# Kernel tuning notes

Hardware: AMD Instinct MI355X
Metric: run time of the kernel (lower is better)

## Reference

```python
import jax, jax.numpy as jnp
import numpy as np

N, D_IN, D_HID, N_EXPERTS, TOP_K = 16384, 2048, 2048, 8, 2


def setup_inputs() -> dict:
    key = jax.random.key(0)
    k1, k2, k3, k4, k5 = jax.random.split(key, 5)
    x = jax.random.normal(k1, (N, D_IN), dtype=jnp.float32)
    W_experts = jax.random.normal(k2, (N_EXPERTS, D_IN, D_HID), dtype=jnp.float32) * 0.02
    b_experts = jax.random.normal(k3, (N_EXPERTS, D_HID), dtype=jnp.float32) * 0.02
    W_gate = jax.random.normal(k4, (D_IN, N_EXPERTS), dtype=jnp.float32) * 0.02
    b_gate = jax.random.normal(k5, (N_EXPERTS,), dtype=jnp.float32) * 0.02
    return {"x": x, "W_experts": W_experts, "b_experts": b_experts,
            "W_gate": W_gate, "b_gate": b_gate}


def reference(x, W_experts, b_experts, W_gate, b_gate):
    # gating softmax over experts: [N, E]
    gates = jax.nn.softmax(x @ W_gate + b_gate, axis=-1)
    # per-token top-k scores/indices: [N, K]
    top_scores, top_idx = jax.lax.top_k(gates, TOP_K)
    # FAITHFUL to original: experts chosen by the FIRST token's indices for all tokens
    idx0 = top_idx[0]                       # [K]
    W_sel = W_experts[idx0]                 # [K, D_IN, D_HID]
    b_sel = b_experts[idx0]                 # [K, D_HID]
    expert_out = jnp.einsum('ni,kio->nko', x, W_sel) + b_sel[None]  # [N, K, D_HID]
    # weight by each token's own top-k scores and sum over the K experts
    return (expert_out * top_scores[:, :, None]).sum(axis=1)        # [N, D_HID]
```

## Files before the change

### kernel.cpp

```cpp
#include <hip/hip_runtime.h>
#include <hip/hip_bf16.h>
#include <stdint.h>

#define N_TOK 16384
#define D_IN  2048
#define D_HID 2048

typedef __attribute__((ext_vector_type(8))) short  bf16x8;
typedef __attribute__((ext_vector_type(4))) float  f32x4;
typedef __attribute__((ext_vector_type(8))) unsigned short u16x8;

__device__ __forceinline__ unsigned short f2bf(float f) {
    unsigned int u = __float_as_uint(f);
    u = (u + 0x7FFFu + ((u >> 16) & 1u)) >> 16;
    return (unsigned short)u;
}

__global__ void gate_kernel(const float* __restrict__ x,
                            const float* __restrict__ Wg,
                            const float* __restrict__ bg,
                            float* __restrict__ s12,
                            int* __restrict__ eidx) {
    const int token = blockIdx.x * 4 + (threadIdx.x >> 6);
    const int lane  = threadIdx.x & 63;
    const float* xr = x + (size_t)token * D_IN;

    float acc[8];
#pragma unroll
    for (int e = 0; e < 8; ++e) acc[e] = 0.f;

    for (int i = lane; i < D_IN; i += 64) {
        float xv = xr[i];
        const float4* wr = (const float4*)(Wg + (size_t)i * 8);
        float4 w0 = wr[0], w1 = wr[1];
        acc[0] += xv * w0.x; acc[1] += xv * w0.y;
        acc[2] += xv * w0.z; acc[3] += xv * w0.w;
        acc[4] += xv * w1.x; acc[5] += xv * w1.y;
        acc[6] += xv * w1.z; acc[7] += xv * w1.w;
    }
#pragma unroll
    for (int off = 32; off > 0; off >>= 1) {
#pragma unroll
        for (int e = 0; e < 8; ++e) acc[e] += __shfl_xor(acc[e], off);
    }

    float lg[8];
    float mx = -1e30f;
#pragma unroll
    for (int e = 0; e < 8; ++e) { lg[e] = acc[e] + bg[e]; mx = fmaxf(mx, lg[e]); }
    float sum = 0.f;
#pragma unroll
    for (int e = 0; e < 8; ++e) { lg[e] = expf(lg[e] - mx); sum += lg[e]; }
    float inv = 1.f / sum;

    float s1 = -1.f, s2 = -1.f; int i1 = 0, i2 = 0;
#pragma unroll
    for (int e = 0; e < 8; ++e) {
        float g = lg[e] * inv;
        if (g > s1)      { s2 = s1; i2 = i1; s1 = g; i1 = e; }
        else if (g > s2) { s2 = g;  i2 = e; }
    }
    if (lane == 0) {
        s12[token * 2]     = s1;
        s12[token * 2 + 1] = s2;
        if (token == 0) { eidx[0] = i1; eidx[1] = i2; }
    }
}

__global__ __launch_bounds__(256) void xconv_kernel(
    const float* __restrict__ x, unsigned short* __restrict__ xb) {
    const int mt = blockIdx.x >> 6;
    const int kt = blockIdx.x & 63;
    const int t  = threadIdx.x;
    const float* src = x + ((size_t)(mt * 256 + t)) * D_IN + kt * 32;
    unsigned short* slab = xb + ((size_t)(mt * 64 + kt)) * 8192;
#pragma unroll
    for (int ks = 0; ks < 4; ++ks) {
        float4 a = *(const float4*)(src + ks * 8);
        float4 b = *(const float4*)(src + ks * 8 + 4);
        u16x8 v;
        v[0] = f2bf(a.x); v[1] = f2bf(a.y); v[2] = f2bf(a.z); v[3] = f2bf(a.w);
        v[4] = f2bf(b.x); v[5] = f2bf(b.y); v[6] = f2bf(b.z); v[7] = f2bf(b.w);
        *(u16x8*)(slab + (ks * 256 + t) * 8) = v;
    }
}

__global__ void wconv_kernel(const float* __restrict__ W,
                             const int* __restrict__ eidx,
                             unsigned short* __restrict__ wbT) {
    __shared__ float tile[64][65];
    const int be  = blockIdx.z;
    const int e   = eidx[be];
    const int k0  = blockIdx.y * 64;
    const int n0  = blockIdx.x * 64;
    const int bx  = n0 >> 7;
    const int cl0 = n0 & 127;
    const int kt0 = k0 >> 5;
    const float* src = W + (size_t)e * D_IN * D_HID;
    const int t = threadIdx.x;

#pragma unroll
    for (int p = 0; p < 4; ++p) {
        int row = p * 16 + (t >> 4);
        int col = (t & 15) * 4;
        const float* s = src + (size_t)(k0 + row) * D_HID + n0 + col;
        tile[row][col]     = s[0];
        tile[row][col + 1] = s[1];
        tile[row][col + 2] = s[2];
        tile[row][col + 3] = s[3];
    }
    __syncthreads();

    const int g   = (t >> 5) * 8;
    const int ktl = t >> 7;
    const int ks  = (t >> 5) & 3;
#pragma unroll
    for (int p = 0; p < 2; ++p) {
        int n = p * 32 + (t & 31);
        u16x8 v;
#pragma unroll
        for (int j = 0; j < 8; ++j) v[j] = f2bf(tile[g + j][n]);
        unsigned short* dst = wbT + ((size_t)(bx * 64 + kt0 + ktl)) * 8192 +
                              ((size_t)(ks * 256 + be * 128 + cl0 + n)) * 8;
        *(u16x8*)dst = v;
    }
}

#define GLD16(gp, lp)                                                        \
    __builtin_amdgcn_global_load_lds(                                        \
        (const __attribute__((address_space(1))) void*)(gp),                 \
        (__attribute__((address_space(3))) void*)(lp), 16, 0, 0)

#define LDSV(SLOT) (*(const bf16x8*)&lds[(SLOT) * 8])

#define STAGE_A(SBAS, KT)                                                    \
    do {                                                                     \
        GLD16(gA0 + (size_t)(KT) * 8192,        &lds[((SBAS) + t512) * 8]);  \
        GLD16(gA0 + (size_t)(KT) * 8192 + 4096, &lds[((SBAS) + 512 + t512) * 8]); \
    } while (0)
#define STAGE_B(SBAS, KT)                                                    \
    do {                                                                     \
        GLD16(gB0 + (size_t)(KT) * 8192,        &lds[((SBAS) + 1024 + t512) * 8]); \
        GLD16(gB0 + (size_t)(KT) * 8192 + 4096, &lds[((SBAS) + 1536 + t512) * 8]); \
    } while (0)

#define MF(MI, AV)                                                                              \
    acc[MI][0] = __builtin_amdgcn_mfma_f32_16x16x32_bf16(AV, bf0, acc[MI][0], 0, 0, 0);         \
    acc[MI][1] = __builtin_amdgcn_mfma_f32_16x16x32_bf16(AV, bf1, acc[MI][1], 0, 0, 0);         \
    acc[MI][2] = __builtin_amdgcn_mfma_f32_16x16x32_bf16(AV, bf2, acc[MI][2], 0, 0, 0);         \
    acc[MI][3] = __builtin_amdgcn_mfma_f32_16x16x32_bf16(AV, bf3, acc[MI][3], 0, 0, 0);

#define TILE(RB, SB, KT, DO_STAGE, VMSTR)                                    \
    do {                                                                     \
        const int rbas  = (RB) * 2048;                                       \
        const int abase = rbas + aks + arow;                                 \
        const int bbase = rbas + 1024 + aks + brow;                          \
        bf16x8 bf0 = LDSV(bbase), bf1 = LDSV(bbase + 16),                    \
               bf2 = LDSV(bbase + 32), bf3 = LDSV(bbase + 48);               \
        bf16x8 a0 = LDSV(abase), a1 = LDSV(abase + 16),                      \
               a2 = LDSV(abase + 32), a3 = LDSV(abase + 48);                 \
        bf16x8 a4 = LDSV(abase + 64), a5 = LDSV(abase + 80),                 \
               a6 = LDSV(abase + 96), a7 = LDSV(abase + 112);                \
        __builtin_amdgcn_s_barrier();                                        \
        if (DO_STAGE) STAGE_A((SB) * 2048, KT);                              \
        __builtin_amdgcn_s_setprio(1);                                       \
        MF(0, a0) MF(1, a1) MF(2, a2) MF(3, a3)                              \
        __builtin_amdgcn_s_setprio(0);                                       \
        asm volatile(VMSTR ::: "memory");                                    \
        __builtin_amdgcn_s_barrier();                                        \
        if (DO_STAGE) STAGE_B((SB) * 2048, KT);                              \
        __builtin_amdgcn_s_setprio(1);                                       \
        MF(4, a4) MF(5, a5) MF(6, a6) MF(7, a7)                              \
        __builtin_amdgcn_s_setprio(0);                                       \
    } while (0)

__global__ __launch_bounds__(512, 2) void moe_gemm_kernel(
    const unsigned short* __restrict__ xb,
    const unsigned short* __restrict__ wbT,
    const float* __restrict__ b_exp,
    const int* __restrict__ eidx,
    const float* __restrict__ s12,
    float* __restrict__ out) {
    __shared__ __align__(16) short lds[4 * 2048 * 8];

    const int t512 = threadIdx.x;
    const int lane = t512 & 63;
    const int w    = t512 >> 6;
    const int wm   = w >> 2;
    const int wn   = w & 3;

    const int bid = blockIdx.x;
    const int xcd = bid & 7;
    const int jb  = bid >> 3;
    const int bx  = xcd * 2 + (jb & 1);
    const int by  = jb >> 1;
    const int mbase = by * 256;
    const int nbase = bx * 128;

    const unsigned short* gA0 = xb  + ((size_t)by * 64) * 8192 + t512 * 8;
    const unsigned short* gB0 = wbT + ((size_t)bx * 64) * 8192 + t512 * 8;

    const int aks  = (lane >> 4) * 256;
    const int arow = wm * 128 + (lane & 15);
    const int brow = wn * 64 + (lane & 15);

    f32x4 acc[8][4];
#pragma unroll
    for (int mi = 0; mi < 8; ++mi)
#pragma unroll
        for (int ni = 0; ni < 4; ++ni) acc[mi][ni] = (f32x4){0.f, 0.f, 0.f, 0.f};

    STAGE_A(0, 0);    STAGE_B(0, 0);
    STAGE_A(2048, 1); STAGE_B(2048, 1);
    STAGE_A(4096, 2); STAGE_B(4096, 2);
    asm volatile("s_waitcnt vmcnt(8)" ::: "memory");
    __builtin_amdgcn_s_barrier();

#pragma unroll 4
    for (int t = 0; t < 61; ++t) {
        TILE(t & 3, (t + 3) & 3, t + 3, 1, "s_waitcnt vmcnt(6)");
    }
    TILE(1, 0, 0, 0, "s_waitcnt vmcnt(4)");
    TILE(2, 0, 0, 0, "s_waitcnt vmcnt(0)");
    TILE(3, 0, 0, 0, "s_waitcnt vmcnt(0)");

    __syncthreads();
    float* fl = (float*)lds;
    if (wn >= 2) {
        float* reg = fl + (wm * 2 + (wn - 2)) * 8192;
#pragma unroll
        for (int mi = 0; mi < 8; ++mi)
#pragma unroll
            for (int ni = 0; ni < 4; ++ni)
#pragma unroll
                for (int j = 0; j < 4; ++j) {
                    int row_l = mi * 16 + ((lane >> 4) << 2) + j;
                    int col_l = ni * 16 + (lane & 15);
                    reg[row_l * 64 + col_l] = acc[mi][ni][j];
                }
    }
    __syncthreads();
    if (wn < 2) {
        const float* reg = fl + (wm * 2 + wn) * 8192;
        const int e0 = eidx[0], e1 = eidx[1];
        const float* bb0 = b_exp + (size_t)e0 * D_HID;
        const float* bb1 = b_exp + (size_t)e1 * D_HID;
        const float2* s12v = (const float2*)s12;
        int   cc[4];
        float b0c[4], b1c[4];
#pragma unroll
        for (int ni = 0; ni < 4; ++ni) {
            cc[ni]  = nbase + wn * 64 + ni * 16 + (lane & 15);
            b0c[ni] = bb0[cc[ni]];
            b1c[ni] = bb1[cc[ni]];
        }
#pragma unroll
        for (int mi = 0; mi < 8; ++mi)
#pragma unroll
            for (int j = 0; j < 4; ++j) {
                int row_l = mi * 16 + ((lane >> 4) << 2) + j;
                int r = mbase + wm * 128 + row_l;
                float2 s = s12v[r];
#pragma unroll
                for (int ni = 0; ni < 4; ++ni) {
                    float y1 = reg[row_l * 64 + ni * 16 + (lane & 15)];
                    out[(size_t)r * D_HID + cc[ni]] =
                        s.x * (acc[mi][ni][j] + b0c[ni]) + s.y * (y1 + b1c[ni]);
                }
            }
    }
}

extern "C" void kernel_launch(void* const* d_in, const int* in_sizes, int n_in,
                              void* d_out, int out_size, void* d_ws, size_t ws_size,
                              hipStream_t stream) {
    const float* x         = (const float*)d_in[0];
    const float* W_experts = (const float*)d_in[1];
    const float* b_experts = (const float*)d_in[2];
    const float* W_gate    = (const float*)d_in[3];
    const float* b_gate    = (const float*)d_in[4];
    float* out = (float*)d_out;

    char* ws = (char*)d_ws;
    float* s12  = (float*)ws;
    int*   eidx = (int*)(ws + 131072);
    unsigned short* xb  = (unsigned short*)(ws + 262144);
    unsigned short* wbT = (unsigned short*)(ws + 262144 + 67108864);

    gate_kernel<<<N_TOK / 4, 256, 0, stream>>>(x, W_gate, b_gate, s12, eidx);
    xconv_kernel<<<4096, 256, 0, stream>>>(x, xb);
    wconv_kernel<<<dim3(32, 32, 2), 256, 0, stream>>>(W_experts, eidx, wbT);
    moe_gemm_kernel<<<1024, 512, 0, stream>>>(xb, wbT, b_experts, eidx, s12, out);
}
```

Baseline: 323.0 us.

## Fuse gating matvec into x conversion and switch GEMM to 32x32x16 MFMA

The gate logits are now computed as per-k-tile partial sums inside the x-to-bf16 conversion kernel, so x is read once instead of twice. A small finishing kernel reduces the partials, applies softmax and top-2, and writes the scores and expert indices; the partials are staged in the output buffer. Separately, the main GEMM inner loop moves from 16x16x32 to 32x32x16 bf16 MFMA with a 4x2 accumulator tile per wave, which cuts LDS fragment loads per FLOP. The epilogue is remapped to the 32x32 accumulator layout. Risks are higher register pressure from the 16-wide accumulators and the extra partial-sum traffic through the output buffer.

```diff
diff --git a/kernel.cpp b/kernel.cpp
--- a/kernel.cpp
+++ b/kernel.cpp
@@ -6,9 +6,9 @@
 #define D_IN  2048
 #define D_HID 2048
 
-typedef __attribute__((ext_vector_type(8))) short  bf16x8;
-typedef __attribute__((ext_vector_type(4))) float  f32x4;
-typedef __attribute__((ext_vector_type(8))) unsigned short u16x8;
+typedef __attribute__((ext_vector_type(8)))  short bf16x8;
+typedef __attribute__((ext_vector_type(16))) float f32x16;
+typedef __attribute__((ext_vector_type(8)))  unsigned short u16x8;
 
 __device__ __forceinline__ unsigned short f2bf(float f) {
     unsigned int u = __float_as_uint(f);
@@ -16,73 +16,73 @@
     return (unsigned short)u;
 }
 
-__global__ void gate_kernel(const float* __restrict__ x,
-                            const float* __restrict__ Wg,
-                            const float* __restrict__ bg,
-                            float* __restrict__ s12,
-                            int* __restrict__ eidx) {
-    const int token = blockIdx.x * 4 + (threadIdx.x >> 6);
-    const int lane  = threadIdx.x & 63;
-    const float* xr = x + (size_t)token * D_IN;
-
-    float acc[8];
-#pragma unroll
-    for (int e = 0; e < 8; ++e) acc[e] = 0.f;
-
-    for (int i = lane; i < D_IN; i += 64) {
-        float xv = xr[i];
-        const float4* wr = (const float4*)(Wg + (size_t)i * 8);
-        float4 w0 = wr[0], w1 = wr[1];
-        acc[0] += xv * w0.x; acc[1] += xv * w0.y;
-        acc[2] += xv * w0.z; acc[3] += xv * w0.w;
-        acc[4] += xv * w1.x; acc[5] += xv * w1.y;
-        acc[6] += xv * w1.z; acc[7] += xv * w1.w;
-    }
-#pragma unroll
-    for (int off = 32; off > 0; off >>= 1) {
-#pragma unroll
-        for (int e = 0; e < 8; ++e) acc[e] += __shfl_xor(acc[e], off);
-    }
-
-    float lg[8];
-    float mx = -1e30f;
-#pragma unroll
-    for (int e = 0; e < 8; ++e) { lg[e] = acc[e] + bg[e]; mx = fmaxf(mx, lg[e]); }
-    float sum = 0.f;
-#pragma unroll
-    for (int e = 0; e < 8; ++e) { lg[e] = expf(lg[e] - mx); sum += lg[e]; }
-    float inv = 1.f / sum;
-
-    float s1 = -1.f, s2 = -1.f; int i1 = 0, i2 = 0;
-#pragma unroll
-    for (int e = 0; e < 8; ++e) {
-        float g = lg[e] * inv;
-        if (g > s1)      { s2 = s1; i2 = i1; s1 = g; i1 = e; }
-        else if (g > s2) { s2 = g;  i2 = e; }
-    }
-    if (lane == 0) {
-        s12[token * 2]     = s1;
-        s12[token * 2 + 1] = s2;
-        if (token == 0) { eidx[0] = i1; eidx[1] = i2; }
-    }
-}
-
-__global__ __launch_bounds__(256) void xconv_kernel(
-    const float* __restrict__ x, unsigned short* __restrict__ xb) {
+__global__ __launch_bounds__(256) void xconv2_kernel(
+    const float* __restrict__ x, const float* __restrict__ Wg,
+    unsigned short* __restrict__ xb, float* __restrict__ part) {
     const int mt = blockIdx.x >> 6;
     const int kt = blockIdx.x & 63;
     const int t  = threadIdx.x;
     const float* src = x + ((size_t)(mt * 256 + t)) * D_IN + kt * 32;
     unsigned short* slab = xb + ((size_t)(mt * 64 + kt)) * 8192;
+    const float* wg = Wg + kt * 32 * 8;
+
+    float p[8];
+#pragma unroll
+    for (int e = 0; e < 8; ++e) p[e] = 0.f;
+
 #pragma unroll
     for (int ks = 0; ks < 4; ++ks) {
         float4 a = *(const float4*)(src + ks * 8);
         float4 b = *(const float4*)(src + ks * 8 + 4);
+        float xv[8] = {a.x, a.y, a.z, a.w, b.x, b.y, b.z, b.w};
         u16x8 v;
-        v[0] = f2bf(a.x); v[1] = f2bf(a.y); v[2] = f2bf(a.z); v[3] = f2bf(a.w);
-        v[4] = f2bf(b.x); v[5] = f2bf(b.y); v[6] = f2bf(b.z); v[7] = f2bf(b.w);
+#pragma unroll
+        for (int j = 0; j < 8; ++j) v[j] = f2bf(xv[j]);
         *(u16x8*)(slab + (ks * 256 + t) * 8) = v;
-    }
+#pragma unroll
+        for (int j = 0; j < 8; ++j)
+#pragma unroll
+            for (int e = 0; e < 8; ++e)
+                p[e] += xv[j] * wg[(ks * 8 + j) * 8 + e];
+    }
+    float* dst = part + (((size_t)(mt * 64 + kt)) * 256 + t) * 8;
+#pragma unroll
+    for (int e = 0; e < 8; ++e) dst[e] = p[e];
+}
+
+__global__ __launch_bounds__(256) void gatefin_kernel(
+    const float* __restrict__ part, const float* __restrict__ bg,
+    float* __restrict__ s12, int* __restrict__ eidx) {
+    const int mt = blockIdx.x;
+    const int t  = threadIdx.x;
+    float l8[8];
+#pragma unroll
+    for (int e = 0; e < 8; ++e) l8[e] = 0.f;
+    for (int kt = 0; kt < 64; ++kt) {
+        const float* pp = part + (((size_t)(mt * 64 + kt)) * 256 + t) * 8;
+        float4 a = *(const float4*)pp;
+        float4 b = *(const float4*)(pp + 4);
+        l8[0] += a.x; l8[1] += a.y; l8[2] += a.z; l8[3] += a.w;
+        l8[4] += b.x; l8[5] += b.y; l8[6] += b.z; l8[7] += b.w;
+    }
+    float mx = -1e30f;
+#pragma unroll
+    for (int e = 0; e < 8; ++e) { l8[e] += bg[e]; mx = fmaxf(mx, l8[e]); }
+    float sum = 0.f;
+#pragma unroll
+    for (int e = 0; e < 8; ++e) { l8[e] = expf(l8[e] - mx); sum += l8[e]; }
+    float inv = 1.f / sum;
+    float s1 = -1.f, s2 = -1.f; int i1 = 0, i2 = 0;
+#pragma unroll
+    for (int e = 0; e < 8; ++e) {
+        float g = l8[e] * inv;
+        if (g > s1)      { s2 = s1; i2 = i1; s1 = g; i1 = e; }
+        else if (g > s2) { s2 = g;  i2 = e; }
+    }
+    const int token = mt * 256 + t;
+    s12[token * 2]     = s1;
+    s12[token * 2 + 1] = s2;
+    if (token == 0) { eidx[0] = i1; eidx[1] = i2; }
 }
 
 __global__ void wconv_kernel(const float* __restrict__ W,
@@ -144,33 +144,37 @@
         GLD16(gB0 + (size_t)(KT) * 8192 + 4096, &lds[((SBAS) + 1536 + t512) * 8]); \
     } while (0)
 
-#define MF(MI, AV)                                                                              \
-    acc[MI][0] = __builtin_amdgcn_mfma_f32_16x16x32_bf16(AV, bf0, acc[MI][0], 0, 0, 0);         \
-    acc[MI][1] = __builtin_amdgcn_mfma_f32_16x16x32_bf16(AV, bf1, acc[MI][1], 0, 0, 0);         \
-    acc[MI][2] = __builtin_amdgcn_mfma_f32_16x16x32_bf16(AV, bf2, acc[MI][2], 0, 0, 0);         \
-    acc[MI][3] = __builtin_amdgcn_mfma_f32_16x16x32_bf16(AV, bf3, acc[MI][3], 0, 0, 0);
+#define MFC(KK)                                                              \
+    _Pragma("unroll")                                                        \
+    for (int mi = 0; mi < 4; ++mi)                                           \
+        _Pragma("unroll")                                                    \
+        for (int ni = 0; ni < 2; ++ni)                                       \
+            acc[mi][ni] = __builtin_amdgcn_mfma_f32_32x32x16_bf16(           \
+                af[KK][mi], bf[KK][ni], acc[mi][ni], 0, 0, 0);
 
 #define TILE(RB, SB, KT, DO_STAGE, VMSTR)                                    \
     do {                                                                     \
-        const int rbas  = (RB) * 2048;                                       \
-        const int abase = rbas + aks + arow;                                 \
-        const int bbase = rbas + 1024 + aks + brow;                          \
-        bf16x8 bf0 = LDSV(bbase), bf1 = LDSV(bbase + 16),                    \
-               bf2 = LDSV(bbase + 32), bf3 = LDSV(bbase + 48);               \
-        bf16x8 a0 = LDSV(abase), a1 = LDSV(abase + 16),                      \
-               a2 = LDSV(abase + 32), a3 = LDSV(abase + 48);                 \
-        bf16x8 a4 = LDSV(abase + 64), a5 = LDSV(abase + 80),                 \
-               a6 = LDSV(abase + 96), a7 = LDSV(abase + 112);                \
+        const int rbas = (RB) * 2048;                                        \
+        bf16x8 af[2][4], bf[2][2];                                           \
+        _Pragma("unroll")                                                    \
+        for (int kk = 0; kk < 2; ++kk) {                                     \
+            _Pragma("unroll")                                                \
+            for (int ni = 0; ni < 2; ++ni)                                   \
+                bf[kk][ni] = LDSV(rbas + 1024 + kk * 512 + bbase + ni * 32); \
+            _Pragma("unroll")                                                \
+            for (int mi = 0; mi < 4; ++mi)                                   \
+                af[kk][mi] = LDSV(rbas + kk * 512 + abase + mi * 32);        \
+        }                                                                    \
         __builtin_amdgcn_s_barrier();                                        \
         if (DO_STAGE) STAGE_A((SB) * 2048, KT);                              \
         __builtin_amdgcn_s_setprio(1);                                       \
-        MF(0, a0) MF(1, a1) MF(2, a2) MF(3, a3)                              \
+        MFC(0)                                                               \
         __builtin_amdgcn_s_setprio(0);                                       \
         asm volatile(VMSTR ::: "memory");                                    \
         __builtin_amdgcn_s_barrier();                                        \
         if (DO_STAGE) STAGE_B((SB) * 2048, KT);                              \
         __builtin_amdgcn_s_setprio(1);                                       \
-        MF(4, a4) MF(5, a5) MF(6, a6) MF(7, a7)                              \
+        MFC(1)                                                               \
         __builtin_amdgcn_s_setprio(0);                                       \
     } while (0)
 
@@ -188,6 +192,8 @@
     const int w    = t512 >> 6;
     const int wm   = w >> 2;
     const int wn   = w & 3;
+    const int lsk  = lane >> 5;
+    const int lr   = lane & 31;
 
     const int bid = blockIdx.x;
     const int xcd = bid & 7;
@@ -200,15 +206,16 @@
     const unsigned short* gA0 = xb  + ((size_t)by * 64) * 8192 + t512 * 8;
     const unsigned short* gB0 = wbT + ((size_t)bx * 64) * 8192 + t512 * 8;
 
-    const int aks  = (lane >> 4) * 256;
-    const int arow = wm * 128 + (lane & 15);
-    const int brow = wn * 64 + (lane & 15);
-
-    f32x4 acc[8][4];
-#pragma unroll
-    for (int mi = 0; mi < 8; ++mi)
-#pragma unroll
-        for (int ni = 0; ni < 4; ++ni) acc[mi][ni] = (f32x4){0.f, 0.f, 0.f, 0.f};
+    const int abase = lsk * 256 + wm * 128 + lr;
+    const int bbase = lsk * 256 + wn * 64 + lr;
+
+    f32x16 acc[4][2];
+#pragma unroll
+    for (int mi = 0; mi < 4; ++mi)
+#pragma unroll
+        for (int ni = 0; ni < 2; ++ni)
+#pragma unroll
+            for (int r = 0; r < 16; ++r) acc[mi][ni][r] = 0.f;
 
     STAGE_A(0, 0);    STAGE_B(0, 0);
     STAGE_A(2048, 1); STAGE_B(2048, 1);
@@ -229,14 +236,13 @@
     if (wn >= 2) {
         float* reg = fl + (wm * 2 + (wn - 2)) * 8192;
 #pragma unroll
-        for (int mi = 0; mi < 8; ++mi)
-#pragma unroll
-            for (int ni = 0; ni < 4; ++ni)
-#pragma unroll
-                for (int j = 0; j < 4; ++j) {
-                    int row_l = mi * 16 + ((lane >> 4) << 2) + j;
-                    int col_l = ni * 16 + (lane & 15);
-                    reg[row_l * 64 + col_l] = acc[mi][ni][j];
+        for (int mi = 0; mi < 4; ++mi)
+#pragma unroll
+            for (int ni = 0; ni < 2; ++ni)
+#pragma unroll
+                for (int r = 0; r < 16; ++r) {
+                    int row_l = mi * 32 + (r & 3) + 8 * (r >> 2) + 4 * lsk;
+                    reg[row_l * 64 + ni * 32 + lr] = acc[mi][ni][r];
                 }
     }
     __syncthreads();
@@ -246,26 +252,26 @@
         const float* bb0 = b_exp + (size_t)e0 * D_HID;
         const float* bb1 = b_exp + (size_t)e1 * D_HID;
         const float2* s12v = (const float2*)s12;
-        int   cc[4];
-        float b0c[4], b1c[4];
-#pragma unroll
-        for (int ni = 0; ni < 4; ++ni) {
-            cc[ni]  = nbase + wn * 64 + ni * 16 + (lane & 15);
+        int   cc[2];
+        float b0c[2], b1c[2];
+#pragma unroll
+        for (int ni = 0; ni < 2; ++ni) {
+            cc[ni]  = nbase + wn * 64 + ni * 32 + lr;
             b0c[ni] = bb0[cc[ni]];
             b1c[ni] = bb1[cc[ni]];
         }
 #pragma unroll
-        for (int mi = 0; mi < 8; ++mi)
-#pragma unroll
-            for (int j = 0; j < 4; ++j) {
-                int row_l = mi * 16 + ((lane >> 4) << 2) + j;
-                int r = mbase + wm * 128 + row_l;
-                float2 s = s12v[r];
-#pragma unroll
-                for (int ni = 0; ni < 4; ++ni) {
-                    float y1 = reg[row_l * 64 + ni * 16 + (lane & 15)];
-                    out[(size_t)r * D_HID + cc[ni]] =
-                        s.x * (acc[mi][ni][j] + b0c[ni]) + s.y * (y1 + b1c[ni]);
+        for (int mi = 0; mi < 4; ++mi)
+#pragma unroll
+            for (int r = 0; r < 16; ++r) {
+                int row_l = mi * 32 + (r & 3) + 8 * (r >> 2) + 4 * lsk;
+                int rg = mbase + wm * 128 + row_l;
+                float2 s = s12v[rg];
+#pragma unroll
+                for (int ni = 0; ni < 2; ++ni) {
+                    float y1 = reg[row_l * 64 + ni * 32 + lr];
+                    out[(size_t)rg * D_HID + cc[ni]] =
+                        s.x * (acc[mi][ni][r] + b0c[ni]) + s.y * (y1 + b1c[ni]);
                 }
             }
     }
@@ -286,9 +292,10 @@
     int*   eidx = (int*)(ws + 131072);
     unsigned short* xb  = (unsigned short*)(ws + 262144);
     unsigned short* wbT = (unsigned short*)(ws + 262144 + 67108864);
-
-    gate_kernel<<<N_TOK / 4, 256, 0, stream>>>(x, W_gate, b_gate, s12, eidx);
-    xconv_kernel<<<4096, 256, 0, stream>>>(x, xb);
+    float* part = out;
+
+    xconv2_kernel<<<4096, 256, 0, stream>>>(x, W_gate, xb, part);
+    gatefin_kernel<<<64, 256, 0, stream>>>(part, b_gate, s12, eidx);
     wconv_kernel<<<dim3(32, 32, 2), 256, 0, stream>>>(W_experts, eidx, wbT);
     moe_gemm_kernel<<<1024, 512, 0, stream>>>(xb, wbT, b_experts, eidx, s12, out);
 }
```

After: 316.8 us. About the same (-1.9%).

## Fuse gating matvec into x bf16 conversion pass with split-K partials

Applied to the files above, without the earlier changes.

The gate logits are now computed as split-K partial dot products inside the kernel that already reads x to convert it to bf16, so x is read from memory once instead of twice. The partials go into a scratch buffer that aliases the output tensor, and a small second kernel sums them and does the softmax and top-2. This removes a full fp32 read of x (about 128 MB) but writes and rereads 32 MB of partials, and the finish kernel runs on only 64 blocks. The per-thread inner product also adds many gate-weight loads and FMAs to the conversion kernel.

```diff
diff --git a/kernel.cpp b/kernel.cpp
--- a/kernel.cpp
+++ b/kernel.cpp
@@ -16,73 +16,73 @@
     return (unsigned short)u;
 }
 
-__global__ void gate_kernel(const float* __restrict__ x,
-                            const float* __restrict__ Wg,
-                            const float* __restrict__ bg,
-                            float* __restrict__ s12,
-                            int* __restrict__ eidx) {
-    const int token = blockIdx.x * 4 + (threadIdx.x >> 6);
-    const int lane  = threadIdx.x & 63;
-    const float* xr = x + (size_t)token * D_IN;
-
-    float acc[8];
-#pragma unroll
-    for (int e = 0; e < 8; ++e) acc[e] = 0.f;
-
-    for (int i = lane; i < D_IN; i += 64) {
-        float xv = xr[i];
-        const float4* wr = (const float4*)(Wg + (size_t)i * 8);
-        float4 w0 = wr[0], w1 = wr[1];
-        acc[0] += xv * w0.x; acc[1] += xv * w0.y;
-        acc[2] += xv * w0.z; acc[3] += xv * w0.w;
-        acc[4] += xv * w1.x; acc[5] += xv * w1.y;
-        acc[6] += xv * w1.z; acc[7] += xv * w1.w;
-    }
-#pragma unroll
-    for (int off = 32; off > 0; off >>= 1) {
-#pragma unroll
-        for (int e = 0; e < 8; ++e) acc[e] += __shfl_xor(acc[e], off);
-    }
-
-    float lg[8];
-    float mx = -1e30f;
-#pragma unroll
-    for (int e = 0; e < 8; ++e) { lg[e] = acc[e] + bg[e]; mx = fmaxf(mx, lg[e]); }
-    float sum = 0.f;
-#pragma unroll
-    for (int e = 0; e < 8; ++e) { lg[e] = expf(lg[e] - mx); sum += lg[e]; }
-    float inv = 1.f / sum;
-
-    float s1 = -1.f, s2 = -1.f; int i1 = 0, i2 = 0;
-#pragma unroll
-    for (int e = 0; e < 8; ++e) {
-        float g = lg[e] * inv;
-        if (g > s1)      { s2 = s1; i2 = i1; s1 = g; i1 = e; }
-        else if (g > s2) { s2 = g;  i2 = e; }
-    }
-    if (lane == 0) {
-        s12[token * 2]     = s1;
-        s12[token * 2 + 1] = s2;
-        if (token == 0) { eidx[0] = i1; eidx[1] = i2; }
-    }
-}
-
-__global__ __launch_bounds__(256) void xconv_kernel(
-    const float* __restrict__ x, unsigned short* __restrict__ xb) {
+__global__ __launch_bounds__(256) void xconv2_kernel(
+    const float* __restrict__ x, const float* __restrict__ Wg,
+    unsigned short* __restrict__ xb, float* __restrict__ part) {
     const int mt = blockIdx.x >> 6;
     const int kt = blockIdx.x & 63;
     const int t  = threadIdx.x;
     const float* src = x + ((size_t)(mt * 256 + t)) * D_IN + kt * 32;
     unsigned short* slab = xb + ((size_t)(mt * 64 + kt)) * 8192;
+    const float* wg = Wg + kt * 32 * 8;
+
+    float p[8];
+#pragma unroll
+    for (int e = 0; e < 8; ++e) p[e] = 0.f;
+
 #pragma unroll
     for (int ks = 0; ks < 4; ++ks) {
         float4 a = *(const float4*)(src + ks * 8);
         float4 b = *(const float4*)(src + ks * 8 + 4);
+        float xv[8] = {a.x, a.y, a.z, a.w, b.x, b.y, b.z, b.w};
         u16x8 v;
-        v[0] = f2bf(a.x); v[1] = f2bf(a.y); v[2] = f2bf(a.z); v[3] = f2bf(a.w);
-        v[4] = f2bf(b.x); v[5] = f2bf(b.y); v[6] = f2bf(b.z); v[7] = f2bf(b.w);
+#pragma unroll
+        for (int j = 0; j < 8; ++j) v[j] = f2bf(xv[j]);
         *(u16x8*)(slab + (ks * 256 + t) * 8) = v;
-    }
+#pragma unroll
+        for (int j = 0; j < 8; ++j)
+#pragma unroll
+            for (int e = 0; e < 8; ++e)
+                p[e] += xv[j] * wg[(ks * 8 + j) * 8 + e];
+    }
+    float* dst = part + (((size_t)(mt * 64 + kt)) * 256 + t) * 8;
+#pragma unroll
+    for (int e = 0; e < 8; ++e) dst[e] = p[e];
+}
+
+__global__ __launch_bounds__(256) void gatefin_kernel(
+    const float* __restrict__ part, const float* __restrict__ bg,
+    float* __restrict__ s12, int* __restrict__ eidx) {
+    const int mt = blockIdx.x;
+    const int t  = threadIdx.x;
+    float l8[8];
+#pragma unroll
+    for (int e = 0; e < 8; ++e) l8[e] = 0.f;
+    for (int kt = 0; kt < 64; ++kt) {
+        const float* pp = part + (((size_t)(mt * 64 + kt)) * 256 + t) * 8;
+        float4 a = *(const float4*)pp;
+        float4 b = *(const float4*)(pp + 4);
+        l8[0] += a.x; l8[1] += a.y; l8[2] += a.z; l8[3] += a.w;
+        l8[4] += b.x; l8[5] += b.y; l8[6] += b.z; l8[7] += b.w;
+    }
+    float mx = -1e30f;
+#pragma unroll
+    for (int e = 0; e < 8; ++e) { l8[e] += bg[e]; mx = fmaxf(mx, l8[e]); }
+    float sum = 0.f;
+#pragma unroll
+    for (int e = 0; e < 8; ++e) { l8[e] = expf(l8[e] - mx); sum += l8[e]; }
+    float inv = 1.f / sum;
+    float s1 = -1.f, s2 = -1.f; int i1 = 0, i2 = 0;
+#pragma unroll
+    for (int e = 0; e < 8; ++e) {
+        float g = l8[e] * inv;
+        if (g > s1)      { s2 = s1; i2 = i1; s1 = g; i1 = e; }
+        else if (g > s2) { s2 = g;  i2 = e; }
+    }
+    const int token = mt * 256 + t;
+    s12[token * 2]     = s1;
+    s12[token * 2 + 1] = s2;
+    if (token == 0) { eidx[0] = i1; eidx[1] = i2; }
 }
 
 __global__ void wconv_kernel(const float* __restrict__ W,
@@ -286,9 +286,10 @@
     int*   eidx = (int*)(ws + 131072);
     unsigned short* xb  = (unsigned short*)(ws + 262144);
     unsigned short* wbT = (unsigned short*)(ws + 262144 + 67108864);
-
-    gate_kernel<<<N_TOK / 4, 256, 0, stream>>>(x, W_gate, b_gate, s12, eidx);
-    xconv_kernel<<<4096, 256, 0, stream>>>(x, xb);
+    float* part = out;
+
+    xconv2_kernel<<<4096, 256, 0, stream>>>(x, W_gate, xb, part);
+    gatefin_kernel<<<64, 256, 0, stream>>>(part, b_gate, s12, eidx);
     wconv_kernel<<<dim3(32, 32, 2), 256, 0, stream>>>(W_experts, eidx, wbT);
     moe_gemm_kernel<<<1024, 512, 0, stream>>>(xb, wbT, b_experts, eidx, s12, out);
 }
```

Result: faster. 296.9 us (-8.1%).
